# Kernel tuning notes

Hardware: AMD Instinct MI355X
Metric: run time of the kernel (lower is better)

## Reference

```python
import jax, jax.numpy as jnp
import numpy as np

HIDDEN = 2048
N_HEADS = 32
N_KV_HEADS = 8
HEAD_DIM = HIDDEN // N_HEADS  # 64
N_GROUPS = N_HEADS // N_KV_HEADS  # 4
EPS = 1e-6
BATCH = 2
SEQ = 2048


def setup_inputs() -> dict:
    key = jax.random.key(0)
    ks = jax.random.split(key, 8)
    s = 1.0 / np.sqrt(HIDDEN)
    return {
        "hidden_states": jax.random.normal(ks[0], (BATCH, SEQ, HIDDEN), jnp.float32),
        # torch nn.Linear weights: [out_features, in_features]
        "Wq": jax.random.normal(ks[1], (N_HEADS * HEAD_DIM, HIDDEN), jnp.float32) * s,
        "Wk": jax.random.normal(ks[2], (N_KV_HEADS * HEAD_DIM, HIDDEN), jnp.float32) * s,
        "Wv": jax.random.normal(ks[3], (N_KV_HEADS * HEAD_DIM, HIDDEN), jnp.float32) * s,
        "Wo": jax.random.normal(ks[4], (HIDDEN, N_HEADS * HEAD_DIM), jnp.float32) * s,
        "q_norm_weight": jnp.ones((HEAD_DIM,), jnp.float32),
        "k_norm_weight": jnp.ones((HEAD_DIM,), jnp.float32),
    }


def _rmsnorm(x, w, eps=EPS):
    # x: [..., head_dim]
    rms = jax.lax.rsqrt(jnp.mean(x * x, axis=-1, keepdims=True) + eps)
    return x * rms * w


def reference(hidden_states, Wq, Wk, Wv, Wo, q_norm_weight, k_norm_weight):
    B, S, _ = hidden_states.shape
    # projections (y = x @ W.T)
    q = jnp.einsum('bsh,oh->bso', hidden_states, Wq)
    k = jnp.einsum('bsh,oh->bso', hidden_states, Wk)
    v = jnp.einsum('bsh,oh->bso', hidden_states, Wv)
    # [B, H, S, D]
    q = q.reshape(B, S, N_HEADS, HEAD_DIM).transpose(0, 2, 1, 3)
    k = k.reshape(B, S, N_KV_HEADS, HEAD_DIM).transpose(0, 2, 1, 3)
    v = v.reshape(B, S, N_KV_HEADS, HEAD_DIM).transpose(0, 2, 1, 3)
    # GQA repeat_interleave along head dim
    k = jnp.repeat(k, N_GROUPS, axis=1)
    v = jnp.repeat(v, N_GROUPS, axis=1)
    # fused QK RMSNorm
    q = _rmsnorm(q, q_norm_weight)
    k = _rmsnorm(k, k_norm_weight)
    # scaled dot-product attention with causal mask
    scale = 1.0 / np.sqrt(HEAD_DIM)
    scores = jnp.einsum('bhqd,bhkd->bhqk', q, k) * scale
    causal = jnp.tril(jnp.ones((S, S), dtype=bool))
    scores = jnp.where(causal, scores, jnp.finfo(scores.dtype).min)
    attn = jax.nn.softmax(scores, axis=-1)
    out = jnp.einsum('bhqk,bhkd->bhqd', attn, v)  # [B, H, S, D]
    out = out.transpose(0, 2, 1, 3).reshape(B, S, N_HEADS * HEAD_DIM)
    return jnp.einsum('bso,ho->bsh', out, Wo)
```

## Files before the change

### kernel.cpp

```cpp
#include <hip/hip_runtime.h>

typedef _Float16 f16;
typedef _Float16 f16x8 __attribute__((ext_vector_type(8)));
typedef _Float16 f16x4 __attribute__((ext_vector_type(4)));
typedef __fp16 fp16x2 __attribute__((ext_vector_type(2)));
typedef float f32x4 __attribute__((ext_vector_type(4)));

#define HID 2048
#define NH 32
#define NKV 8
#define HD 64
#define SEQ 2048
#define NB 2

__device__ __forceinline__ void gload_lds16(const void* g, void* l) {
  __builtin_amdgcn_global_load_lds((const __attribute__((address_space(1))) void*)g,
                                   (__attribute__((address_space(3))) void*)l, 16, 0, 0);
}

__device__ __forceinline__ uint cvt_pk_f16(float a, float b) {
  auto v = __builtin_amdgcn_cvt_pkrtz(a, b);
  uint u;
  __builtin_memcpy(&u, &v, 4);
  return u;
}

__device__ __forceinline__ float fdot2_ones(uint pk, float acc) {
  fp16x2 a;
  __builtin_memcpy(&a, &pk, 4);
  fp16x2 ones = {(__fp16)1.0f, (__fp16)1.0f};
  return __builtin_amdgcn_fdot2(a, ones, acc, false);
}

__global__ __launch_bounds__(256) void cvt_all(const float* __restrict__ X,
                                               const float* __restrict__ Wq,
                                               const float* __restrict__ Wk,
                                               const float* __restrict__ Wv,
                                               const float* __restrict__ Wo,
                                               f16* __restrict__ Xb, f16* __restrict__ Wqb,
                                               f16* __restrict__ Wkb, f16* __restrict__ Wvb,
                                               f16* __restrict__ Wob) {
  long i = (long)blockIdx.x * 256 + threadIdx.x;
  const float* s; f16* d; long o;
  if (i < 2097152)      { s = X;  d = Xb;  o = i; }
  else if (i < 3145728) { s = Wq; d = Wqb; o = i - 2097152; }
  else if (i < 3407872) { s = Wk; d = Wkb; o = i - 3145728; }
  else if (i < 3670016) { s = Wv; d = Wvb; o = i - 3407872; }
  else                  { s = Wo; d = Wob; o = i - 3670016; }
  float4 v = ((const float4*)s)[o];
  f16x4 ov = { (f16)v.x, (f16)v.y, (f16)v.z, (f16)v.w };
  ((f16x4*)d)[o] = ov;
}

template <typename CT>
__global__ __launch_bounds__(256) void gemm_bt(const f16* __restrict__ A,
                                               const f16* __restrict__ Bm,
                                               CT* __restrict__ C0, CT* __restrict__ C1,
                                               int M, int N, int K,
                                               int n_split, int ldc0, int ldc1) {
  __shared__ f16 As[2][128 * 64];
  __shared__ f16 Bs[2][128 * 64];
  const int t = threadIdx.x;
  const int lane = t & 63;
  const int w = t >> 6;
  const int wr = w >> 1, wc = w & 1;
  const int g = lane >> 4;
  const int lr = lane & 15;

  const int nwg = gridDim.x * gridDim.y;
  const int orig = blockIdx.y * gridDim.x + blockIdx.x;
  const int wg = (orig & 7) * (nwg >> 3) + (orig >> 3);
  const int m0 = (wg / gridDim.x) * 128;
  const int n0 = (wg % gridDim.x) * 128;

  f32x4 acc[4][4] = {};

  const int nkt = K / 64;

  auto stage = [&](int buf, int kt) {
    const int k0 = kt * 64;
#pragma unroll
    for (int i = 0; i < 4; ++i) {
      int c = w * 4 + i;
      int o = c * 1024 + lane * 16;
      int row = o >> 7;
      int ss = ((o >> 4) & 7) ^ (row & 7);
      const char* srcA = (const char*)A + ((size_t)(m0 + row) * K + k0) * 2 + ss * 16;
      gload_lds16(srcA, (char*)(&As[buf][0]) + c * 1024);
      const char* srcB = (const char*)Bm + ((size_t)(n0 + row) * K + k0) * 2 + ss * 16;
      gload_lds16(srcB, (char*)(&Bs[buf][0]) + c * 1024);
    }
  };

  stage(0, 0);
  if (nkt > 1) stage(1, 1);
  for (int kt = 0; kt < nkt; ++kt) {
    const int cur = kt & 1;
    if (kt + 1 < nkt) asm volatile("s_waitcnt vmcnt(8)" ::: "memory");
    else              asm volatile("s_waitcnt vmcnt(0)" ::: "memory");
    __builtin_amdgcn_s_barrier();
    __builtin_amdgcn_sched_barrier(0);

    f16x8 af[2][4], bf[2][4];
#pragma unroll
    for (int ks = 0; ks < 2; ++ks)
#pragma unroll
      for (int mf = 0; mf < 4; ++mf) {
        int row = wr * 64 + mf * 16 + lr;
        int slot = (g + 4 * ks) ^ (row & 7);
        af[ks][mf] = *(const f16x8*)((const char*)(&As[cur][0]) + row * 128 + slot * 16);
      }
#pragma unroll
    for (int ks = 0; ks < 2; ++ks)
#pragma unroll
      for (int nf = 0; nf < 4; ++nf) {
        int row = wc * 64 + nf * 16 + lr;
        int slot = (g + 4 * ks) ^ (row & 7);
        bf[ks][nf] = *(const f16x8*)((const char*)(&Bs[cur][0]) + row * 128 + slot * 16);
      }
    asm volatile("s_waitcnt lgkmcnt(0)" ::: "memory");
    __builtin_amdgcn_sched_barrier(0);
    __builtin_amdgcn_s_barrier();

    if (kt + 2 < nkt) stage(cur, kt + 2);

    __builtin_amdgcn_s_setprio(1);
#pragma unroll
    for (int ks = 0; ks < 2; ++ks)
#pragma unroll
      for (int mf = 0; mf < 4; ++mf)
#pragma unroll
        for (int nf = 0; nf < 4; ++nf)
          acc[mf][nf] = __builtin_amdgcn_mfma_f32_16x16x32_f16(af[ks][mf], bf[ks][nf], acc[mf][nf], 0, 0, 0);
    __builtin_amdgcn_s_setprio(0);
  }

  CT* Cp; int ldc, nb;
  if (n0 < n_split) { Cp = C0; ldc = ldc0; nb = n0; }
  else              { Cp = C1; ldc = ldc1; nb = n0 - n_split; }
#pragma unroll
  for (int mf = 0; mf < 4; ++mf)
#pragma unroll
    for (int nf = 0; nf < 4; ++nf)
#pragma unroll
      for (int r = 0; r < 4; ++r) {
        int mm = m0 + wr * 64 + mf * 16 + g * 4 + r;
        int nn = nb + wc * 64 + nf * 16 + lr;
        Cp[(size_t)mm * ldc + nn] = (CT)acc[mf][nf][r];
      }
}

__global__ __launch_bounds__(256) void rmsnorm_all(f16* __restrict__ Qb,
                                                   f16* __restrict__ KVb,
                                                   const float* __restrict__ qw,
                                                   const float* __restrict__ kw) {
  int c = blockIdx.x * 4 + (threadIdx.x >> 6);
  int lane = threadIdx.x & 63;
  f16* base; const float* w; float extra;
  if (c < 131072) {
    base = Qb + (size_t)(c >> 5) * 2048 + (c & 31) * 64;
    w = qw; extra = 0.125f;
  } else {
    int c2 = c - 131072;
    base = KVb + (size_t)(c2 >> 3) * 1024 + (c2 & 7) * 64;
    w = kw; extra = 1.0f;
  }
  float x = (float)base[lane];
  float ss = x * x;
#pragma unroll
  for (int d = 1; d < 64; d <<= 1) ss += __shfl_xor(ss, d);
  float sc = rsqrtf(ss * (1.0f / 64.0f) + 1e-6f) * extra;
  base[lane] = (f16)(x * sc * w[lane]);
}

__global__ __launch_bounds__(256) void vtrans(const f16* __restrict__ KV,
                                              f16* __restrict__ VT) {
  __shared__ f16 tile[64][72];
  int t = threadIdx.x;
  int st = blockIdx.x, hk = blockIdx.y, b = blockIdx.z;
#pragma unroll
  for (int p = 0; p < 2; ++p) {
    int idx = p * 256 + t;
    int s = idx >> 3, c8 = (idx & 7) * 8;
    f16x8 v = *(const f16x8*)(KV + (size_t)(b * SEQ + st * 64 + s) * 1024 + 512 + hk * 64 + c8);
    *(f16x8*)(&tile[s][c8]) = v;
  }
  __syncthreads();
#pragma unroll
  for (int p = 0; p < 2; ++p) {
    int idx = p * 256 + t;
    int d = idx >> 3, s8 = (idx & 7) * 8;
    f16x8 ov;
#pragma unroll
    for (int j = 0; j < 8; ++j) ov[j] = tile[s8 + j][d];
    *(f16x8*)(VT + ((size_t)((b * NKV + hk) * 64) + d) * SEQ + st * 64 + s8) = ov;
  }
}

__global__ __launch_bounds__(512) void attn(const f16* __restrict__ Q,
                                            const f16* __restrict__ KV,
                                            const f16* __restrict__ VT,
                                            f16* __restrict__ AO) {
  __shared__ f16 Ks[3][64 * 64];
  __shared__ f16 Vs[3][64 * 64];
  const int t = threadIdx.x, lane = t & 63, w = t >> 6;
  const int g = lane >> 4, lr = lane & 15;
  const int col = blockIdx.x;
  const int qt = 31 - blockIdx.y;
  const int b = col & 1;
  const int h = 2 * (col >> 1) + (w >> 2);
  const int rg = w & 3;
  const int hk = h >> 2;
  const int q0 = qt * 64;

  const size_t qrow = (size_t)(b * SEQ + q0 + rg * 16 + lr);
  f16x8 qf[2];
  qf[0] = *(const f16x8*)(Q + qrow * HID + h * 64 + g * 8);
  qf[1] = *(const f16x8*)(Q + qrow * HID + h * 64 + g * 8 + 32);

  int koff[2][4], vlo[2][4], vhi[2][4];
#pragma unroll
  for (int ks = 0; ks < 2; ++ks)
#pragma unroll
    for (int nf = 0; nf < 4; ++nf) {
      int row = nf * 16 + lr;
      koff[ks][nf] = row * 128 + (((g + 4 * ks) ^ (row & 7)) * 16);
    }
#pragma unroll
  for (int m = 0; m < 2; ++m)
#pragma unroll
    for (int df = 0; df < 4; ++df) {
      int row = df * 16 + lr;
      int base = row * 128 + (g & 1) * 8;
      vlo[m][df] = base + (((4 * m + (g >> 1)) ^ (row & 7)) * 16);
      vhi[m][df] = base + (((4 * m + 2 + (g >> 1)) ^ (row & 7)) * 16);
    }

  f32x4 oacc[4] = {};
  float psum0 = 0.0f, psum1 = 0.0f;

  const int nkt = qt + 1;

  auto stage = [&](int buf, int kt2) {
    int o = w * 1024 + lane * 16;
    int row = o >> 7;
    int ss = ((o >> 4) & 7) ^ (row & 7);
    gload_lds16((const char*)KV + ((size_t)(b * SEQ + kt2 * 64 + row) * 1024 + hk * 64) * 2 + ss * 16,
                (char*)(&Ks[buf][0]) + w * 1024);
    gload_lds16((const char*)VT + (((size_t)((b * NKV + hk) * 64) + row) * SEQ + kt2 * 64) * 2 + ss * 16,
                (char*)(&Vs[buf][0]) + w * 1024);
  };

  stage(0, 0);
  if (nkt > 1) stage(1, 1);
  int cur = 0;
  for (int kt = 0; kt < nkt; ++kt) {
    if (kt + 1 < nkt) asm volatile("s_waitcnt vmcnt(2)" ::: "memory");
    else              asm volatile("s_waitcnt vmcnt(0)" ::: "memory");
    __builtin_amdgcn_s_barrier();
    asm volatile("" ::: "memory");

    if (kt + 2 < nkt) {
      int nb = cur + 2; if (nb >= 3) nb -= 3;
      stage(nb, kt + 2);
    }

    const char* Kb = (const char*)(&Ks[cur][0]);
    const char* Vb = (const char*)(&Vs[cur][0]);

    f32x4 sacc[4] = {};
#pragma unroll
    for (int ks = 0; ks < 2; ++ks) {
      __builtin_amdgcn_s_setprio(1);
#pragma unroll
      for (int nf = 0; nf < 4; ++nf) {
        f16x8 kf = *(const f16x8*)(Kb + koff[ks][nf]);
        sacc[nf] = __builtin_amdgcn_mfma_f32_16x16x32_f16(kf, qf[ks], sacc[nf], 0, 0, 0);
      }
      __builtin_amdgcn_s_setprio(0);
    }

    if (kt == qt) {
      int qq = q0 + rg * 16 + lr;
#pragma unroll
      for (int nf = 0; nf < 4; ++nf) {
        int kvb = kt * 64 + nf * 16 + g * 4;
#pragma unroll
        for (int r = 0; r < 4; ++r)
          if (kvb + r > qq) sacc[nf][r] = -1e30f;
      }
    }

    uint pk[8];
#pragma unroll
    for (int nf = 0; nf < 4; ++nf) {
      float p0 = __expf(sacc[nf][0]);
      float p1 = __expf(sacc[nf][1]);
      float p2 = __expf(sacc[nf][2]);
      float p3 = __expf(sacc[nf][3]);
      pk[2 * nf]     = cvt_pk_f16(p0, p1);
      pk[2 * nf + 1] = cvt_pk_f16(p2, p3);
      psum0 = fdot2_ones(pk[2 * nf], psum0);
      psum1 = fdot2_ones(pk[2 * nf + 1], psum1);
    }

#pragma unroll
    for (int m = 0; m < 2; ++m) {
      union { uint u[4]; f16x8 v; } pu;
      pu.u[0] = pk[4 * m];     pu.u[1] = pk[4 * m + 1];
      pu.u[2] = pk[4 * m + 2]; pu.u[3] = pk[4 * m + 3];
      __builtin_amdgcn_s_setprio(1);
#pragma unroll
      for (int df = 0; df < 4; ++df) {
        union { f16x4 h[2]; f16x8 v; } vu;
        vu.h[0] = *(const f16x4*)(Vb + vlo[m][df]);
        vu.h[1] = *(const f16x4*)(Vb + vhi[m][df]);
        oacc[df] = __builtin_amdgcn_mfma_f32_16x16x32_f16(pu.v, vu.v, oacc[df], 0, 0, 0);
      }
      __builtin_amdgcn_s_setprio(0);
    }

    cur = (cur == 2) ? 0 : cur + 1;
  }

  float psum = psum0 + psum1;
  psum += __shfl_xor(psum, 16);
  psum += __shfl_xor(psum, 32);
  float pdiv[4];
#pragma unroll
  for (int r = 0; r < 4; ++r) pdiv[r] = __shfl(psum, g * 4 + r);

#pragma unroll
  for (int df = 0; df < 4; ++df)
#pragma unroll
    for (int r = 0; r < 4; ++r) {
      size_t rowg = (size_t)(b * SEQ + q0 + rg * 16 + g * 4 + r);
      AO[rowg * HID + h * 64 + df * 16 + lr] = (f16)(oacc[df][r] / pdiv[r]);
    }
}

extern "C" void kernel_launch(void* const* d_in, const int* in_sizes, int n_in,
                              void* d_out, int out_size, void* d_ws, size_t ws_size,
                              hipStream_t stream) {
  const float* X  = (const float*)d_in[0];
  const float* Wq = (const float*)d_in[1];
  const float* Wk = (const float*)d_in[2];
  const float* Wv = (const float*)d_in[3];
  const float* Wo = (const float*)d_in[4];
  const float* qw = (const float*)d_in[5];
  const float* kw = (const float*)d_in[6];

  char* ws = (char*)d_ws;
  f16* Xb   = (f16*)(ws + 0);
  f16* Wqkv = (f16*)(ws + 16777216);
  f16* Wob  = (f16*)(ws + 29360128);
  f16* Qb   = (f16*)(ws + 37748736);
  f16* KVb  = (f16*)(ws + 54525952);
  f16* VTb  = (f16*)(ws + 62914560);
  f16* AOb  = (f16*)(ws + 67108864);
  float* OUT = (float*)d_out;

  cvt_all<<<18432, 256, 0, stream>>>(X, Wq, Wk, Wv, Wo,
                                     Xb, Wqkv, Wqkv + 2048 * 2048, Wqkv + 2560 * 2048, Wob);

  gemm_bt<f16><<<dim3(24, 32), 256, 0, stream>>>(Xb, Wqkv, Qb, KVb,
                                                 4096, 3072, 2048, 2048, 2048, 1024);

  rmsnorm_all<<<40960, 256, 0, stream>>>(Qb, KVb, qw, kw);

  vtrans<<<dim3(32, 8, 2), 256, 0, stream>>>(KVb, VTb);
  attn<<<dim3(32, 32, 1), 512, 0, stream>>>(Qb, KVb, VTb, AOb);

  gemm_bt<float><<<dim3(16, 32), 256, 0, stream>>>(AOb, Wob, OUT, OUT,
                                                   4096, 2048, 2048, 2048, 2048, 2048);
}
```

Measured before the change: 192.2 us.

## Fuse QK RMSNorm into V-transpose and attention kernels, permute V layout

Drops the standalone rmsnorm kernel. K is normalized in place inside the V-transpose kernel and Q is normalized in registers when it is loaded in the attention kernel. This removes a kernel launch and a full read/write pass over Q and K. The V-transpose now writes keys in a permuted order so the attention kernel can fetch each V fragment with one 16-byte LDS read instead of two 8-byte reads. The price is extra per-block normalization work in the attention kernel and a layout dependency between the two kernels.

```diff
diff --git a/kernel.cpp b/kernel.cpp
--- a/kernel.cpp
+++ b/kernel.cpp
@@ -150,34 +150,30 @@
       }
 }
 
-__global__ __launch_bounds__(256) void rmsnorm_all(f16* __restrict__ Qb,
-                                                   f16* __restrict__ KVb,
-                                                   const float* __restrict__ qw,
-                                                   const float* __restrict__ kw) {
-  int c = blockIdx.x * 4 + (threadIdx.x >> 6);
-  int lane = threadIdx.x & 63;
-  f16* base; const float* w; float extra;
-  if (c < 131072) {
-    base = Qb + (size_t)(c >> 5) * 2048 + (c & 31) * 64;
-    w = qw; extra = 0.125f;
-  } else {
-    int c2 = c - 131072;
-    base = KVb + (size_t)(c2 >> 3) * 1024 + (c2 & 7) * 64;
-    w = kw; extra = 1.0f;
-  }
-  float x = (float)base[lane];
-  float ss = x * x;
-#pragma unroll
-  for (int d = 1; d < 64; d <<= 1) ss += __shfl_xor(ss, d);
-  float sc = rsqrtf(ss * (1.0f / 64.0f) + 1e-6f) * extra;
-  base[lane] = (f16)(x * sc * w[lane]);
-}
-
-__global__ __launch_bounds__(256) void vtrans(const f16* __restrict__ KV,
-                                              f16* __restrict__ VT) {
+__global__ __launch_bounds__(256) void vtrans(f16* __restrict__ KV,
+                                              f16* __restrict__ VT,
+                                              const float* __restrict__ kw) {
   __shared__ f16 tile[64][72];
   int t = threadIdx.x;
   int st = blockIdx.x, hk = blockIdx.y, b = blockIdx.z;
+
+#pragma unroll
+  for (int p = 0; p < 2; ++p) {
+    int idx = p * 256 + t;
+    int s = idx >> 3, c8 = (idx & 7) * 8;
+    f16* kp = KV + (size_t)(b * SEQ + st * 64 + s) * 1024 + hk * 64 + c8;
+    f16x8 kv = *(const f16x8*)kp;
+    float ss = 0.f;
+#pragma unroll
+    for (int j = 0; j < 8; ++j) { float x = (float)kv[j]; ss += x * x; }
+    ss += __shfl_xor(ss, 1); ss += __shfl_xor(ss, 2); ss += __shfl_xor(ss, 4);
+    float sc = rsqrtf(ss * (1.0f / 64.0f) + 1e-6f);
+    f16x8 on;
+#pragma unroll
+    for (int j = 0; j < 8; ++j) on[j] = (f16)((float)kv[j] * sc * kw[c8 + j]);
+    *(f16x8*)kp = on;
+  }
+
 #pragma unroll
   for (int p = 0; p < 2; ++p) {
     int idx = p * 256 + t;
@@ -192,7 +188,12 @@
     int d = idx >> 3, s8 = (idx & 7) * 8;
     f16x8 ov;
 #pragma unroll
-    for (int j = 0; j < 8; ++j) ov[j] = tile[s8 + j][d];
+    for (int j = 0; j < 8; ++j) {
+      int pos = s8 + j;
+      int k = (pos & 32) | (((pos >> 2) & 1) << 4) | (((pos >> 4) & 1) << 3)
+            | (((pos >> 3) & 1) << 2) | (pos & 3);
+      ov[j] = tile[k][d];
+    }
     *(f16x8*)(VT + ((size_t)((b * NKV + hk) * 64) + d) * SEQ + st * 64 + s8) = ov;
   }
 }
@@ -200,7 +201,8 @@
 __global__ __launch_bounds__(512) void attn(const f16* __restrict__ Q,
                                             const f16* __restrict__ KV,
                                             const f16* __restrict__ VT,
-                                            f16* __restrict__ AO) {
+                                            f16* __restrict__ AO,
+                                            const float* __restrict__ qw) {
   __shared__ f16 Ks[3][64 * 64];
   __shared__ f16 Vs[3][64 * 64];
   const int t = threadIdx.x, lane = t & 63, w = t >> 6;
@@ -218,7 +220,36 @@
   qf[0] = *(const f16x8*)(Q + qrow * HID + h * 64 + g * 8);
   qf[1] = *(const f16x8*)(Q + qrow * HID + h * 64 + g * 8 + 32);
 
-  int koff[2][4], vlo[2][4], vhi[2][4];
+  {
+    float ss = 0.f;
+#pragma unroll
+    for (int i = 0; i < 2; ++i)
+#pragma unroll
+      for (int j = 0; j < 8; ++j) { float x = (float)qf[i][j]; ss += x * x; }
+    ss += __shfl_xor(ss, 16); ss += __shfl_xor(ss, 32);
+    float sc = rsqrtf(ss * (1.0f / 64.0f) + 1e-6f) * 0.125f;
+    const float4* qw4 = (const float4*)qw;
+    float4 w0 = qw4[2 * g], w1 = qw4[2 * g + 1];
+    float4 w2 = qw4[2 * g + 8], w3 = qw4[2 * g + 9];
+    qf[0][0] = (f16)((float)qf[0][0] * sc * w0.x);
+    qf[0][1] = (f16)((float)qf[0][1] * sc * w0.y);
+    qf[0][2] = (f16)((float)qf[0][2] * sc * w0.z);
+    qf[0][3] = (f16)((float)qf[0][3] * sc * w0.w);
+    qf[0][4] = (f16)((float)qf[0][4] * sc * w1.x);
+    qf[0][5] = (f16)((float)qf[0][5] * sc * w1.y);
+    qf[0][6] = (f16)((float)qf[0][6] * sc * w1.z);
+    qf[0][7] = (f16)((float)qf[0][7] * sc * w1.w);
+    qf[1][0] = (f16)((float)qf[1][0] * sc * w2.x);
+    qf[1][1] = (f16)((float)qf[1][1] * sc * w2.y);
+    qf[1][2] = (f16)((float)qf[1][2] * sc * w2.z);
+    qf[1][3] = (f16)((float)qf[1][3] * sc * w2.w);
+    qf[1][4] = (f16)((float)qf[1][4] * sc * w3.x);
+    qf[1][5] = (f16)((float)qf[1][5] * sc * w3.y);
+    qf[1][6] = (f16)((float)qf[1][6] * sc * w3.z);
+    qf[1][7] = (f16)((float)qf[1][7] * sc * w3.w);
+  }
+
+  int koff[2][4], voff[2][4];
 #pragma unroll
   for (int ks = 0; ks < 2; ++ks)
 #pragma unroll
@@ -231,9 +262,7 @@
 #pragma unroll
     for (int df = 0; df < 4; ++df) {
       int row = df * 16 + lr;
-      int base = row * 128 + (g & 1) * 8;
-      vlo[m][df] = base + (((4 * m + (g >> 1)) ^ (row & 7)) * 16);
-      vhi[m][df] = base + (((4 * m + 2 + (g >> 1)) ^ (row & 7)) * 16);
+      voff[m][df] = row * 128 + (((4 * m + g) ^ (row & 7)) * 16);
     }
 
   f32x4 oacc[4] = {};
@@ -312,10 +341,8 @@
       __builtin_amdgcn_s_setprio(1);
 #pragma unroll
       for (int df = 0; df < 4; ++df) {
-        union { f16x4 h[2]; f16x8 v; } vu;
-        vu.h[0] = *(const f16x4*)(Vb + vlo[m][df]);
-        vu.h[1] = *(const f16x4*)(Vb + vhi[m][df]);
-        oacc[df] = __builtin_amdgcn_mfma_f32_16x16x32_f16(pu.v, vu.v, oacc[df], 0, 0, 0);
+        f16x8 vf = *(const f16x8*)(Vb + voff[m][df]);
+        oacc[df] = __builtin_amdgcn_mfma_f32_16x16x32_f16(pu.v, vf, oacc[df], 0, 0, 0);
       }
       __builtin_amdgcn_s_setprio(0);
     }
@@ -366,10 +393,8 @@
   gemm_bt<f16><<<dim3(24, 32), 256, 0, stream>>>(Xb, Wqkv, Qb, KVb,
                                                  4096, 3072, 2048, 2048, 2048, 1024);
 
-  rmsnorm_all<<<40960, 256, 0, stream>>>(Qb, KVb, qw, kw);
-
-  vtrans<<<dim3(32, 8, 2), 256, 0, stream>>>(KVb, VTb);
-  attn<<<dim3(32, 32, 1), 512, 0, stream>>>(Qb, KVb, VTb, AOb);
+  vtrans<<<dim3(32, 8, 2), 256, 0, stream>>>(KVb, VTb, kw);
+  attn<<<dim3(32, 32, 1), 512, 0, stream>>>(Qb, KVb, VTb, AOb, qw);
 
   gemm_bt<float><<<dim3(16, 32), 256, 0, stream>>>(AOb, Wob, OUT, OUT,
                                                    4096, 2048, 2048, 2048, 2048, 2048);
```

New measurement: 169.3 us. -11.9%, faster.
